# Kernel optimization log

Measured on AMD Instinct MI355X. Metric: run time of the kernel, lower is better.

## Reference

```python
import jax, jax.numpy as jnp
import numpy as np

B, T, C, H = 8, 2048, 768, 768

def setup_inputs() -> dict:
    key = jax.random.key(0)
    ks = jax.random.split(key, 7)
    s = 1.0 / np.sqrt(C)
    return {
        "visual_token": jax.random.normal(ks[0], (B, T, C), dtype=jnp.float32),
        "Wk": jax.random.normal(ks[1], (H, C), dtype=jnp.float32) * s,
        "bk": jax.random.normal(ks[2], (H,), dtype=jnp.float32) * s,
        "Wq": jax.random.normal(ks[3], (H, C), dtype=jnp.float32) * s,
        "bq": jax.random.normal(ks[4], (H,), dtype=jnp.float32) * s,
        "W1": jax.random.normal(ks[5], (C, C), dtype=jnp.float32) * s,
        "W2": jax.random.normal(ks[6], (C, C), dtype=jnp.float32) * s,
    }

def reference(visual_token, Wk, bk, Wq, bq, W1, W2):
    x = visual_token
    k = jnp.einsum('btc,hc->bth', x, Wk) + bk          # [B,T,H]
    q = jnp.einsum('btc,hc->bth', x, Wq) + bq          # [B,T,H]
    scores = jnp.einsum('bih,bjh->bij', k, q)          # K @ Q^T, unscaled
    attn = jax.nn.softmax(scores, axis=1)              # NOTE: softmax over dim=1 as in source
    p = x + jnp.einsum('bij,bjc->bic', attn, x)        # residual with value = input
    h = jnp.einsum('btc,dc->btd', p, W1)               # f_1 (no bias)
    h = jnp.einsum('btd,ed->bte', h, W2)               # f_2 (no bias)
    return p + jax.nn.relu(h)
```

## Files before the change

### kernel.cpp

```cpp
#include <hip/hip_runtime.h>

typedef float    f32x4 __attribute__((ext_vector_type(4)));
typedef _Float16 f16x8 __attribute__((ext_vector_type(8)));
typedef _Float16 f16x4 __attribute__((ext_vector_type(4)));

__device__ __forceinline__ void gload16(const void* g, void* l) {
  __builtin_amdgcn_global_load_lds(
      (__attribute__((address_space(1))) void*)(const void*)g,
      (__attribute__((address_space(3))) void*)l,
      16, 0, 0);
}

__device__ __forceinline__ void bounce_flush(const _Float16* lds, _Float16* gbase,
                                             int ldo, int t) {
#pragma unroll
  for (int it = 0; it < 8; ++it) {
    const int s = t + it * 512;
    const int R = s >> 5;
    const int C = (s & 31) * 8;
    const int wsrc = ((R >> 6) << 2) | (C >> 6);
    const f16x8 v = *(const f16x8*)(lds + wsrc * 4096 + (R & 63) * 64 +
                                    ((C & 63) ^ ((R & 12) << 2)));
    *(f16x8*)(gbase + (size_t)R * ldo + C) = v;
  }
}

template <int EPI>
__global__ __launch_bounds__(512, 4) void gemm_kt(
    const _Float16* __restrict__ A, size_t sA, int lda,
    const _Float16* __restrict__ B, size_t sB, int ldb,
    float* __restrict__ out0, _Float16* __restrict__ out1,
    float* __restrict__ out2,
    size_t sO, int ldo,
    const float* __restrict__ bias,
    const float* __restrict__ resid,
    const _Float16* __restrict__ residh,
    const _Float16* __restrict__ cf,
    int K) {
  __shared__ _Float16 lds[3 * 12288];
  __shared__ _Float16 clds[(EPI == 6) ? 4096 : 1];

  const int gx = gridDim.x, gy = gridDim.y;
  const int nblk = gx * gy * gridDim.z;
  int lin = (blockIdx.z * gy + blockIdx.y) * gx + blockIdx.x;
  lin = (lin & 7) * (nblk >> 3) + (lin >> 3);
  const int b  = lin / (gx * gy);
  const int r2 = lin - b * gx * gy;
  const int m0 = (r2 / gx) * 128;
  const int n0 = (r2 - (r2 / gx) * gx) * 256;

  const int t = threadIdx.x, lane = t & 63, w = t >> 6;
  const int wr = w >> 2;
  const int wc = w & 3;
  const int lr = lane & 15, lq = lane >> 4;

  const _Float16* Ab = A + (size_t)b * sA;
  const _Float16* Bb = B + (size_t)b * sB;

  const int arow = t >> 2;
  const int acol = ((t & 3) ^ ((arow >> 1) & 3)) * 8;
  const _Float16* a_src  = Ab + (size_t)(m0 + arow) * lda + acol;
  const _Float16* b_src0 = Bb + (size_t)(n0 + arow) * ldb + acol;
  const _Float16* b_src1 = b_src0 + (size_t)128 * ldb;
  const int a_dst  = t * 8;
  const int b_dst0 = 4096 + t * 8;
  const int b_dst1 = 4096 + (t + 512) * 8;

  const int swz  = ((lr >> 1) & 3) << 3;
  const int koff = (lq * 8) ^ swz;
  const int a_rd = (wr * 64 + lr) * 32 + koff;
  const int b_rd = 4096 + (wc * 64 + lr) * 32 + koff;

  f32x4 acc[4][4];
#pragma unroll
  for (int f = 0; f < 4; ++f)
#pragma unroll
    for (int j = 0; j < 4; ++j) acc[f][j] = (f32x4){0.f, 0.f, 0.f, 0.f};

  const int NT = K >> 5;

  if constexpr (EPI == 6)
    gload16(cf + ((size_t)b * 32 + (m0 >> 6)) * 2048 + t * 8, clds + t * 8);
  gload16(a_src,       lds + a_dst);
  gload16(b_src0,      lds + b_dst0);
  gload16(b_src1,      lds + b_dst1);
  gload16(a_src  + 32, lds + 12288 + a_dst);
  gload16(b_src0 + 32, lds + 12288 + b_dst0);
  gload16(b_src1 + 32, lds + 12288 + b_dst1);

  int buf = 0;
  for (int kt = 0; kt < NT; ++kt) {
    if (kt + 1 < NT) asm volatile("s_waitcnt vmcnt(3)" ::: "memory");
    else             asm volatile("s_waitcnt vmcnt(0)" ::: "memory");
    __builtin_amdgcn_s_barrier();
    __builtin_amdgcn_sched_barrier(0);

    const _Float16* lb = lds + buf * 12288;
    const int nb = (buf + 2 >= 3) ? buf - 1 : buf + 2;
    _Float16* ln = lds + nb * 12288;

    f16x8 af[4], bf[4], cv;
    if constexpr (EPI == 6)
      cv = *(const f16x8*)(clds + wr * 2048 + kt * 32 + lq * 8);
#pragma unroll
    for (int f = 0; f < 4; ++f) {
      af[f] = *(const f16x8*)(lb + a_rd + f * 512);
      if constexpr (EPI == 6) af[f] = af[f] * cv;
    }
#pragma unroll
    for (int j = 0; j < 4; ++j) bf[j] = *(const f16x8*)(lb + b_rd + j * 512);
    if (kt + 2 < NT) {
      const int ko = (kt + 2) * 32;
      gload16(a_src  + ko, ln + a_dst);
      gload16(b_src0 + ko, ln + b_dst0);
      gload16(b_src1 + ko, ln + b_dst1);
    }
    __builtin_amdgcn_s_setprio(1);
#pragma unroll
    for (int f = 0; f < 4; ++f)
#pragma unroll
      for (int j = 0; j < 4; ++j)
        acc[f][j] = __builtin_amdgcn_mfma_f32_16x16x32_f16(af[f], bf[j], acc[f][j], 0, 0, 0);
    __builtin_amdgcn_s_setprio(0);
    __builtin_amdgcn_sched_barrier(0);
    buf = (buf + 1 >= 3) ? 0 : buf + 1;
  }

  if constexpr (EPI == 0 || EPI == 4 || EPI == 6) {
    __syncthreads();
    _Float16* breg = lds + w * 4096;
    if constexpr (EPI == 4) {
#pragma unroll
      for (int j = 0; j < 4; ++j) {
        float m = -3.4e38f;
#pragma unroll
        for (int f = 0; f < 4; ++f)
#pragma unroll
          for (int r = 0; r < 4; ++r) m = fmaxf(m, acc[f][j][r]);
#pragma unroll
        for (int d = 16; d <= 32; d <<= 1) m = fmaxf(m, __shfl_xor(m, d, 64));
        float Z = 0.f;
        const int cb = ((j ^ lq) << 4) + lr;
#pragma unroll
        for (int f = 0; f < 4; ++f)
#pragma unroll
          for (int r = 0; r < 4; ++r) {
            const _Float16 eh = (_Float16)__expf(acc[f][j][r] - m);
            breg[(f * 16 + lq * 4 + r) * 64 + cb] = eh;
            Z += (float)eh;
          }
#pragma unroll
        for (int d = 16; d <= 32; d <<= 1) Z += __shfl_xor(Z, d, 64);
        if (lq == 0) {
          const int chunk = (m0 >> 6) + wr;
          const int col = n0 + wc * 64 + j * 16 + lr;
          const size_t sidx = ((size_t)b * 32 + chunk) * 2048 + col;
          out0[sidx] = m;
          out2[sidx] = Z;
        }
      }
    } else {
#pragma unroll
      for (int f = 0; f < 4; ++f)
#pragma unroll
        for (int j = 0; j < 4; ++j) {
          const int cb = ((j ^ lq) << 4) + lr;
#pragma unroll
          for (int r = 0; r < 4; ++r) {
            float v = acc[f][j][r];
            if constexpr (EPI == 0) {
              if (bias) v += bias[n0 + wc * 64 + j * 16 + lr];
            } else {
              const int row = m0 + wr * 64 + f * 16 + lq * 4 + r;
              const int col = n0 + wc * 64 + j * 16 + lr;
              v += resid[(size_t)b * sO + (size_t)row * ldo + col];
            }
            breg[(f * 16 + lq * 4 + r) * 64 + cb] = (_Float16)v;
          }
        }
    }
    __syncthreads();
    bounce_flush(lds, out1 + (size_t)b * sO + (size_t)m0 * ldo + n0, ldo, t);
  } else {
#pragma unroll
    for (int f = 0; f < 4; ++f)
#pragma unroll
      for (int j = 0; j < 4; ++j)
#pragma unroll
        for (int r = 0; r < 4; ++r) {
          const int row = m0 + wr * 64 + f * 16 + lq * 4 + r;
          const int col = n0 + wc * 64 + j * 16 + lr;
          const size_t oidx = (size_t)b * sO + (size_t)row * ldo + col;
          const float v = acc[f][j][r];
          out0[oidx] = (float)residh[oidx] + (v > 0.f ? v : 0.f);
        }
  }
}

__global__ __launch_bounds__(256) void wconv(
    const float* __restrict__ Wk, const float* __restrict__ Wq,
    const float* __restrict__ W1, const float* __restrict__ W2,
    _Float16* __restrict__ Wkqf, _Float16* __restrict__ W1f,
    _Float16* __restrict__ W2f,
    const float* __restrict__ bk, const float* __restrict__ bq,
    float* __restrict__ bkq) {
  const int by = blockIdx.y;
  const long i = (long)blockIdx.x * 256 + threadIdx.x;
  if (by == 4) {
    if (i < 768) bkq[i] = bk[i];
    else if (i < 1536) bkq[i] = bq[i - 768];
    return;
  }
  const float* in = (by == 0) ? Wk : (by == 1) ? Wq : (by == 2) ? W1 : W2;
  _Float16* outp = (by == 0) ? Wkqf : (by == 1) ? (Wkqf + 589824)
                  : (by == 2) ? W1f : W2f;
  f32x4 v0 = *(const f32x4*)(in + i * 8);
  f32x4 v1 = *(const f32x4*)(in + i * 8 + 4);
  f16x8 o;
  o[0] = (_Float16)v0[0]; o[1] = (_Float16)v0[1]; o[2] = (_Float16)v0[2]; o[3] = (_Float16)v0[3];
  o[4] = (_Float16)v1[0]; o[5] = (_Float16)v1[1]; o[6] = (_Float16)v1[2]; o[7] = (_Float16)v1[3];
  *(f16x8*)(outp + i * 8) = o;
}

__global__ __launch_bounds__(256) void col_final(const float* __restrict__ pm,
                                                 const float* __restrict__ pZ,
                                                 _Float16* __restrict__ c) {
  const int b = blockIdx.z;
  const int col = blockIdx.x * 256 + threadIdx.x;
  float mv[32];
  float m = -3.4e38f;
#pragma unroll
  for (int k = 0; k < 32; ++k) {
    mv[k] = pm[((size_t)b * 32 + k) * 2048 + col];
    m = fmaxf(m, mv[k]);
  }
  float Z = 0.f;
#pragma unroll
  for (int k = 0; k < 32; ++k)
    Z += pZ[((size_t)b * 32 + k) * 2048 + col] * __expf(mv[k] - m);
  const float rZ = 1.f / Z;
#pragma unroll
  for (int k = 0; k < 32; ++k)
    c[((size_t)b * 32 + k) * 2048 + col] = (_Float16)(__expf(mv[k] - m) * rZ);
}

__global__ void xprep(const float* __restrict__ x, _Float16* __restrict__ xf,
                      _Float16* __restrict__ xT) {
  __shared__ float tile[32][33];
  const int b = blockIdx.z;
  const int c0 = blockIdx.x * 32, j0 = blockIdx.y * 32;
  const float* xb = x + (size_t)b * 2048 * 768;
  const int tx = threadIdx.x, ty = threadIdx.y;
#pragma unroll
  for (int dy = 0; dy < 32; dy += 8)
    tile[ty + dy][tx] = xb[(size_t)(j0 + ty + dy) * 768 + c0 + tx];
  __syncthreads();
  {
    const int u = ty * 32 + tx;
    const int row = u >> 3, c4 = (u & 7) * 4;
    f16x4 o;
#pragma unroll
    for (int q = 0; q < 4; ++q) o[q] = (_Float16)tile[row][c4 + q];
    *(f16x4*)(xf + ((size_t)b * 2048 + j0 + row) * 768 + c0 + c4) = o;
  }
  _Float16* xTb = xT + (size_t)b * 768 * 2048;
#pragma unroll
  for (int dy = 0; dy < 32; dy += 8)
    xTb[(size_t)(c0 + ty + dy) * 2048 + j0 + tx] = (_Float16)tile[tx][ty + dy];
}

extern "C" void kernel_launch(void* const* d_in, const int* in_sizes, int n_in,
                              void* d_out, int out_size, void* d_ws, size_t ws_size,
                              hipStream_t stream) {
  const float* x  = (const float*)d_in[0];
  const float* Wk = (const float*)d_in[1];
  const float* bk = (const float*)d_in[2];
  const float* Wq = (const float*)d_in[3];
  const float* bq = (const float*)d_in[4];
  const float* W1 = (const float*)d_in[5];
  const float* W2 = (const float*)d_in[6];
  float* out = (float*)d_out;

  char* ws = (char*)d_ws;
  size_t off = 0;
  auto alloc = [&](size_t bytes) -> char* {
    char* p = ws + off;
    off += (bytes + 255) & ~(size_t)255;
    return p;
  };
  _Float16* xf = (_Float16*)alloc(25165824);
  _Float16* kq = (_Float16*)alloc(50331648);
  _Float16* Wf = (_Float16*)alloc(4718592);
  _Float16* E  = (_Float16*)alloc(67108864);
  _Float16* xT = (_Float16*)alloc(25165824);
  float*    pm = (float*)alloc(2097152);
  float*    pZ = (float*)alloc(2097152);
  float*    bkq  = (float*)alloc(6144);

  _Float16* Wkqf = Wf;
  _Float16* W1f  = Wf + 2 * 589824;
  _Float16* W2f  = Wf + 3 * 589824;
  _Float16* pf16 = kq;
  _Float16* cT   = kq + 12582912;
  _Float16* hf16 = kq + 12582912;

  const size_t sKQ = (size_t)2048 * 1536;
  const size_t sS  = (size_t)2048 * 2048;
  const size_t sKV = (size_t)2048 * 768;

  xprep<<<dim3(24, 64, 8), dim3(32, 8), 0, stream>>>(x, xf, xT);
  wconv<<<dim3(288, 5), 256, 0, stream>>>(Wk, Wq, W1, W2, Wkqf, W1f, W2f,
                                          bk, bq, bkq);

  gemm_kt<0><<<dim3(6, 128, 1), 512, 0, stream>>>(xf, 0, 768, Wkqf, 0, 768,
                                                  nullptr, kq, nullptr, 0, 1536,
                                                  bkq, nullptr, nullptr, nullptr, 768);

  gemm_kt<4><<<dim3(8, 16, 8), 512, 0, stream>>>(kq, sKQ, 1536, kq + 768, sKQ, 1536,
                                                 pm, E, pZ, sS, 2048,
                                                 nullptr, nullptr, nullptr, nullptr, 768);
  col_final<<<dim3(8, 1, 8), 256, 0, stream>>>(pm, pZ, cT);

  gemm_kt<6><<<dim3(3, 16, 8), 512, 0, stream>>>(E, sS, 2048, xT, sKV, 2048,
                                                 nullptr, pf16, nullptr, sKV, 768,
                                                 nullptr, x, nullptr, cT, 2048);

  gemm_kt<0><<<dim3(3, 128, 1), 512, 0, stream>>>(pf16, 0, 768, W1f, 0, 768,
                                                  nullptr, hf16, nullptr, 0, 768,
                                                  nullptr, nullptr, nullptr, nullptr, 768);

  gemm_kt<3><<<dim3(3, 128, 1), 512, 0, stream>>>(hf16, 0, 768, W2f, 0, 768,
                                                  out, nullptr, nullptr, 0, 768,
                                                  nullptr, nullptr, pf16, nullptr, 768);
}
```

Measured before the change: 264.0 us.

## Replace score GEMM with dedicated 256x256-tile kernel with split-phase pipelining

Moves the K·Q^T score GEMM with its fused exp/partial-max/partial-sum epilogue out of the generic 128x256 gemm_kt into a new epass256 kernel that uses 256x256 tiles. Each wave now computes 8x4 MFMA fragments, and the K-loop is split into two halves so LDS fragment loads and global-to-LDS prefetches overlap the MFMAs, with explicit waitcnt and barriers between them. The larger tile raises arithmetic intensity and reduces reloads of K and Q. In exchange it uses more registers and LDS, runs at occupancy 2, and launches only 512 blocks.

```diff
diff --git a/kernel.cpp b/kernel.cpp
--- a/kernel.cpp
+++ b/kernel.cpp
@@ -30,7 +30,6 @@
     const _Float16* __restrict__ A, size_t sA, int lda,
     const _Float16* __restrict__ B, size_t sB, int ldb,
     float* __restrict__ out0, _Float16* __restrict__ out1,
-    float* __restrict__ out2,
     size_t sO, int ldo,
     const float* __restrict__ bias,
     const float* __restrict__ resid,
@@ -50,8 +49,7 @@
   const int n0 = (r2 - (r2 / gx) * gx) * 256;
 
   const int t = threadIdx.x, lane = t & 63, w = t >> 6;
-  const int wr = w >> 2;
-  const int wc = w & 3;
+  const int wr = w >> 2, wc = w & 3;
   const int lr = lane & 15, lq = lane >> 4;
 
   const _Float16* Ab = A + (size_t)b * sA;
@@ -126,59 +124,27 @@
     buf = (buf + 1 >= 3) ? 0 : buf + 1;
   }
 
-  if constexpr (EPI == 0 || EPI == 4 || EPI == 6) {
+  if constexpr (EPI == 0 || EPI == 6) {
     __syncthreads();
     _Float16* breg = lds + w * 4096;
-    if constexpr (EPI == 4) {
+#pragma unroll
+    for (int f = 0; f < 4; ++f)
 #pragma unroll
       for (int j = 0; j < 4; ++j) {
-        float m = -3.4e38f;
-#pragma unroll
-        for (int f = 0; f < 4; ++f)
-#pragma unroll
-          for (int r = 0; r < 4; ++r) m = fmaxf(m, acc[f][j][r]);
-#pragma unroll
-        for (int d = 16; d <= 32; d <<= 1) m = fmaxf(m, __shfl_xor(m, d, 64));
-        float Z = 0.f;
         const int cb = ((j ^ lq) << 4) + lr;
 #pragma unroll
-        for (int f = 0; f < 4; ++f)
-#pragma unroll
-          for (int r = 0; r < 4; ++r) {
-            const _Float16 eh = (_Float16)__expf(acc[f][j][r] - m);
-            breg[(f * 16 + lq * 4 + r) * 64 + cb] = eh;
-            Z += (float)eh;
+        for (int r = 0; r < 4; ++r) {
+          float v = acc[f][j][r];
+          if constexpr (EPI == 0) {
+            if (bias) v += bias[n0 + wc * 64 + j * 16 + lr];
+          } else {
+            const int row = m0 + wr * 64 + f * 16 + lq * 4 + r;
+            const int col = n0 + wc * 64 + j * 16 + lr;
+            v += resid[(size_t)b * sO + (size_t)row * ldo + col];
           }
-#pragma unroll
-        for (int d = 16; d <= 32; d <<= 1) Z += __shfl_xor(Z, d, 64);
-        if (lq == 0) {
-          const int chunk = (m0 >> 6) + wr;
-          const int col = n0 + wc * 64 + j * 16 + lr;
-          const size_t sidx = ((size_t)b * 32 + chunk) * 2048 + col;
-          out0[sidx] = m;
-          out2[sidx] = Z;
+          breg[(f * 16 + lq * 4 + r) * 64 + cb] = (_Float16)v;
         }
       }
-    } else {
-#pragma unroll
-      for (int f = 0; f < 4; ++f)
-#pragma unroll
-        for (int j = 0; j < 4; ++j) {
-          const int cb = ((j ^ lq) << 4) + lr;
-#pragma unroll
-          for (int r = 0; r < 4; ++r) {
-            float v = acc[f][j][r];
-            if constexpr (EPI == 0) {
-              if (bias) v += bias[n0 + wc * 64 + j * 16 + lr];
-            } else {
-              const int row = m0 + wr * 64 + f * 16 + lq * 4 + r;
-              const int col = n0 + wc * 64 + j * 16 + lr;
-              v += resid[(size_t)b * sO + (size_t)row * ldo + col];
-            }
-            breg[(f * 16 + lq * 4 + r) * 64 + cb] = (_Float16)v;
-          }
-        }
-    }
     __syncthreads();
     bounce_flush(lds, out1 + (size_t)b * sO + (size_t)m0 * ldo + n0, ldo, t);
   } else {
@@ -194,6 +160,172 @@
           const float v = acc[f][j][r];
           out0[oidx] = (float)residh[oidx] + (v > 0.f ? v : 0.f);
         }
+  }
+}
+
+__global__ __launch_bounds__(512, 2) void epass256(
+    const _Float16* __restrict__ A, const _Float16* __restrict__ B,
+    float* __restrict__ pm, float* __restrict__ pZ,
+    _Float16* __restrict__ E) {
+  __shared__ _Float16 lds3[3 * 16384];
+
+  const int gx = 8, gy = 8;
+  const int nblk = 512;
+  int lin = (blockIdx.z * gy + blockIdx.y) * gx + blockIdx.x;
+  lin = (lin & 7) * (nblk >> 3) + (lin >> 3);
+  const int b  = lin >> 6;
+  const int r2 = lin & 63;
+  const int m0 = (r2 >> 3) * 256;
+  const int n0 = (r2 & 7) * 256;
+
+  const int t = threadIdx.x, lane = t & 63, w = t >> 6;
+  const int wr = w >> 2, wc = w & 3;
+  const int lr = lane & 15, lq = lane >> 4;
+
+  const _Float16* Ab = A + (size_t)b * 2048 * 1536;
+  const _Float16* Bb = B + (size_t)b * 2048 * 1536;
+
+  const int arow = t >> 2;
+  const int acol = ((t & 3) ^ ((arow >> 1) & 3)) * 8;
+  const _Float16* a_src0 = Ab + (size_t)(m0 + arow) * 1536 + acol;
+  const _Float16* a_src1 = a_src0 + (size_t)128 * 1536;
+  const _Float16* b_src0 = Bb + (size_t)(n0 + arow) * 1536 + acol;
+  const _Float16* b_src1 = b_src0 + (size_t)128 * 1536;
+  const int a_d0 = t * 8, a_d1 = (t + 512) * 8;
+  const int b_d0 = 8192 + t * 8, b_d1 = 8192 + (t + 512) * 8;
+
+  const int swz  = ((lr >> 1) & 3) << 3;
+  const int koff = (lq * 8) ^ swz;
+  const int a_rd = (wr * 128 + lr) * 32 + koff;
+  const int b_rd = 8192 + (wc * 64 + lr) * 32 + koff;
+
+  f32x4 acc[8][4];
+#pragma unroll
+  for (int f = 0; f < 8; ++f)
+#pragma unroll
+    for (int j = 0; j < 4; ++j) acc[f][j] = (f32x4){0.f, 0.f, 0.f, 0.f};
+
+  const int NT = 24;
+
+  gload16(a_src0, lds3 + a_d0);
+  gload16(a_src1, lds3 + a_d1);
+  gload16(b_src0, lds3 + b_d0);
+  gload16(b_src1, lds3 + b_d1);
+  gload16(a_src0 + 32, lds3 + 16384 + a_d0);
+  gload16(a_src1 + 32, lds3 + 16384 + a_d1);
+  gload16(b_src0 + 32, lds3 + 16384 + b_d0);
+  gload16(b_src1 + 32, lds3 + 16384 + b_d1);
+  asm volatile("s_waitcnt vmcnt(4)" ::: "memory");
+  __builtin_amdgcn_s_barrier();
+  __builtin_amdgcn_sched_barrier(0);
+
+  f16x8 afc[4], afb[4], bfc[4], afn[4], bfn[4];
+#pragma unroll
+  for (int f = 0; f < 4; ++f) afc[f] = *(const f16x8*)(lds3 + a_rd + f * 512);
+#pragma unroll
+  for (int j = 0; j < 4; ++j) bfc[j] = *(const f16x8*)(lds3 + b_rd + j * 512);
+
+  for (int kt = 0; kt < NT; ++kt) {
+    const _Float16* lb = lds3 + (kt % 3) * 16384;
+    const _Float16* lnx = lds3 + ((kt + 1) % 3) * 16384;
+    _Float16* lst = lds3 + ((kt + 2) % 3) * 16384;
+    const bool st2 = (kt + 2 < NT), nx = (kt + 1 < NT);
+    const int ko = (kt + 2) * 32;
+
+    if (st2) {
+      gload16(a_src0 + ko, lst + a_d0);
+      gload16(a_src1 + ko, lst + a_d1);
+    }
+#pragma unroll
+    for (int f = 0; f < 4; ++f) afb[f] = *(const f16x8*)(lb + a_rd + (4 + f) * 512);
+    __builtin_amdgcn_s_setprio(1);
+#pragma unroll
+    for (int f = 0; f < 4; ++f)
+#pragma unroll
+      for (int j = 0; j < 4; ++j)
+        acc[f][j] = __builtin_amdgcn_mfma_f32_16x16x32_f16(afc[f], bfc[j], acc[f][j], 0, 0, 0);
+    __builtin_amdgcn_s_setprio(0);
+    asm volatile("s_waitcnt lgkmcnt(0)" ::: "memory");
+    __builtin_amdgcn_s_barrier();
+    __builtin_amdgcn_sched_barrier(0);
+
+    if (st2) {
+      gload16(b_src0 + ko, lst + b_d0);
+      gload16(b_src1 + ko, lst + b_d1);
+    }
+    if (nx) {
+      if (st2) asm volatile("s_waitcnt vmcnt(4)" ::: "memory");
+      else     asm volatile("s_waitcnt vmcnt(0)" ::: "memory");
+      __builtin_amdgcn_sched_barrier(0);
+#pragma unroll
+      for (int f = 0; f < 4; ++f) afn[f] = *(const f16x8*)(lnx + a_rd + f * 512);
+#pragma unroll
+      for (int j = 0; j < 4; ++j) bfn[j] = *(const f16x8*)(lnx + b_rd + j * 512);
+    }
+    __builtin_amdgcn_s_setprio(1);
+#pragma unroll
+    for (int f = 0; f < 4; ++f)
+#pragma unroll
+      for (int j = 0; j < 4; ++j)
+        acc[4 + f][j] = __builtin_amdgcn_mfma_f32_16x16x32_f16(afb[f], bfc[j], acc[4 + f][j], 0, 0, 0);
+    __builtin_amdgcn_s_setprio(0);
+    asm volatile("s_waitcnt lgkmcnt(0)" ::: "memory");
+    __builtin_amdgcn_s_barrier();
+    __builtin_amdgcn_sched_barrier(0);
+    if (nx) {
+#pragma unroll
+      for (int f = 0; f < 4; ++f) afc[f] = afn[f];
+#pragma unroll
+      for (int j = 0; j < 4; ++j) bfc[j] = bfn[j];
+    }
+  }
+
+  _Float16* breg = lds3 + w * 4096;
+#pragma unroll
+  for (int h = 0; h < 2; ++h) {
+    if (h == 1) __syncthreads();
+#pragma unroll
+    for (int j = 0; j < 4; ++j) {
+      float m = -3.4e38f;
+#pragma unroll
+      for (int f = 0; f < 4; ++f)
+#pragma unroll
+        for (int r = 0; r < 4; ++r) m = fmaxf(m, acc[h * 4 + f][j][r]);
+#pragma unroll
+      for (int d = 16; d <= 32; d <<= 1) m = fmaxf(m, __shfl_xor(m, d, 64));
+      float Z = 0.f;
+      const int cb = ((j ^ lq) << 4) + lr;
+#pragma unroll
+      for (int f = 0; f < 4; ++f)
+#pragma unroll
+        for (int r = 0; r < 4; ++r) {
+          const _Float16 eh = (_Float16)__expf(acc[h * 4 + f][j][r] - m);
+          breg[(f * 16 + lq * 4 + r) * 64 + cb] = eh;
+          Z += (float)eh;
+        }
+#pragma unroll
+      for (int d = 16; d <= 32; d <<= 1) Z += __shfl_xor(Z, d, 64);
+      if (lq == 0) {
+        const int chunk = (m0 >> 6) + wr * 2 + h;
+        const int col = n0 + wc * 64 + j * 16 + lr;
+        const size_t sidx = ((size_t)b * 32 + chunk) * 2048 + col;
+        pm[sidx] = m;
+        pZ[sidx] = Z;
+      }
+    }
+    __syncthreads();
+#pragma unroll
+    for (int it = 0; it < 8; ++it) {
+      const int s = t + it * 512;
+      const int Rp = s >> 5;
+      const int C  = (s & 31) * 8;
+      const int wsrc = ((Rp >> 6) << 2) | (C >> 6);
+      const int rl = Rp & 63;
+      const f16x8 v = *(const f16x8*)(lds3 + wsrc * 4096 + rl * 64 +
+                                      ((C & 63) ^ (((rl >> 2) & 3) << 4)));
+      const int grow = m0 + (Rp >> 6) * 128 + h * 64 + rl;
+      *(f16x8*)(E + (size_t)b * 2048 * 2048 + (size_t)grow * 2048 + n0 + C) = v;
+    }
   }
 }
 
@@ -313,23 +445,21 @@
                                           bk, bq, bkq);
 
   gemm_kt<0><<<dim3(6, 128, 1), 512, 0, stream>>>(xf, 0, 768, Wkqf, 0, 768,
-                                                  nullptr, kq, nullptr, 0, 1536,
+                                                  nullptr, kq, 0, 1536,
                                                   bkq, nullptr, nullptr, nullptr, 768);
 
-  gemm_kt<4><<<dim3(8, 16, 8), 512, 0, stream>>>(kq, sKQ, 1536, kq + 768, sKQ, 1536,
-                                                 pm, E, pZ, sS, 2048,
-                                                 nullptr, nullptr, nullptr, nullptr, 768);
+  epass256<<<dim3(8, 8, 8), 512, 0, stream>>>(kq, kq + 768, pm, pZ, E);
   col_final<<<dim3(8, 1, 8), 256, 0, stream>>>(pm, pZ, cT);
 
   gemm_kt<6><<<dim3(3, 16, 8), 512, 0, stream>>>(E, sS, 2048, xT, sKV, 2048,
-                                                 nullptr, pf16, nullptr, sKV, 768,
+                                                 nullptr, pf16, sKV, 768,
                                                  nullptr, x, nullptr, cT, 2048);
 
   gemm_kt<0><<<dim3(3, 128, 1), 512, 0, stream>>>(pf16, 0, 768, W1f, 0, 768,
-                                                  nullptr, hf16, nullptr, 0, 768,
+                                                  nullptr, hf16, 0, 768,
                                                   nullptr, nullptr, nullptr, nullptr, 768);
 
   gemm_kt<3><<<dim3(3, 128, 1), 512, 0, stream>>>(hf16, 0, 768, W2f, 0, 768,
-                                                  out, nullptr, nullptr, 0, 768,
+                                                  out, nullptr, 0, 768,
                                                   nullptr, nullptr, pf16, nullptr, 768);
 }
```

Measured after the change: 266.0 us. Within noise of the previous version (+0.8%).

## Fold Wq^T Wk into one projection and drop bias terms invariant under softmax

Applied to the files above, without the earlier changes.

Rewrites scores = (xWk^T+bk)(xWq^T+bq)^T as x G x^T plus a per-row term u = x·(Wk^T bq), using G = Wq^T Wk precomputed by a small GEMM. Terms that are constant along the softmax axis (dim 1 over rows i), such as those involving bk, are dropped. The KQ projection GEMM shrinks from 1536 to 768 output columns, and the scores GEMM reads xf directly as its B operand. In exchange it adds weight-prep kernels (transpose, G GEMM, wu, u) and changes fp16 rounding, because G is stored in fp16.

```diff
diff --git a/kernel.cpp b/kernel.cpp
--- a/kernel.cpp
+++ b/kernel.cpp
@@ -43,15 +43,14 @@
   const int gx = gridDim.x, gy = gridDim.y;
   const int nblk = gx * gy * gridDim.z;
   int lin = (blockIdx.z * gy + blockIdx.y) * gx + blockIdx.x;
-  lin = (lin & 7) * (nblk >> 3) + (lin >> 3);
+  if (!(nblk & 7)) lin = (lin & 7) * (nblk >> 3) + (lin >> 3);
   const int b  = lin / (gx * gy);
   const int r2 = lin - b * gx * gy;
   const int m0 = (r2 / gx) * 128;
   const int n0 = (r2 - (r2 / gx) * gx) * 256;
 
   const int t = threadIdx.x, lane = t & 63, w = t >> 6;
-  const int wr = w >> 2;
-  const int wc = w & 3;
+  const int wr = w >> 2, wc = w & 3;
   const int lr = lane & 15, lq = lane >> 4;
 
   const _Float16* Ab = A + (size_t)b * sA;
@@ -130,13 +129,19 @@
     __syncthreads();
     _Float16* breg = lds + w * 4096;
     if constexpr (EPI == 4) {
+      float uu[4][4];
+#pragma unroll
+      for (int f = 0; f < 4; ++f)
+#pragma unroll
+        for (int r = 0; r < 4; ++r)
+          uu[f][r] = bias[(size_t)b * 2048 + m0 + wr * 64 + f * 16 + lq * 4 + r];
 #pragma unroll
       for (int j = 0; j < 4; ++j) {
         float m = -3.4e38f;
 #pragma unroll
         for (int f = 0; f < 4; ++f)
 #pragma unroll
-          for (int r = 0; r < 4; ++r) m = fmaxf(m, acc[f][j][r]);
+          for (int r = 0; r < 4; ++r) m = fmaxf(m, acc[f][j][r] + uu[f][r]);
 #pragma unroll
         for (int d = 16; d <= 32; d <<= 1) m = fmaxf(m, __shfl_xor(m, d, 64));
         float Z = 0.f;
@@ -145,7 +150,7 @@
         for (int f = 0; f < 4; ++f)
 #pragma unroll
           for (int r = 0; r < 4; ++r) {
-            const _Float16 eh = (_Float16)__expf(acc[f][j][r] - m);
+            const _Float16 eh = (_Float16)__expf(acc[f][j][r] + uu[f][r] - m);
             breg[(f * 16 + lq * 4 + r) * 64 + cb] = eh;
             Z += (float)eh;
           }
@@ -197,29 +202,72 @@
   }
 }
 
-__global__ __launch_bounds__(256) void wconv(
-    const float* __restrict__ Wk, const float* __restrict__ Wq,
-    const float* __restrict__ W1, const float* __restrict__ W2,
-    _Float16* __restrict__ Wkqf, _Float16* __restrict__ W1f,
-    _Float16* __restrict__ W2f,
-    const float* __restrict__ bk, const float* __restrict__ bq,
-    float* __restrict__ bkq) {
-  const int by = blockIdx.y;
+__global__ __launch_bounds__(256) void wconv(const float* __restrict__ W1,
+                                             const float* __restrict__ W2,
+                                             _Float16* __restrict__ W1f,
+                                             _Float16* __restrict__ W2f) {
   const long i = (long)blockIdx.x * 256 + threadIdx.x;
-  if (by == 4) {
-    if (i < 768) bkq[i] = bk[i];
-    else if (i < 1536) bkq[i] = bq[i - 768];
-    return;
-  }
-  const float* in = (by == 0) ? Wk : (by == 1) ? Wq : (by == 2) ? W1 : W2;
-  _Float16* outp = (by == 0) ? Wkqf : (by == 1) ? (Wkqf + 589824)
-                  : (by == 2) ? W1f : W2f;
+  const float* in = blockIdx.y ? W2 : W1;
+  _Float16* outp  = blockIdx.y ? W2f : W1f;
   f32x4 v0 = *(const f32x4*)(in + i * 8);
   f32x4 v1 = *(const f32x4*)(in + i * 8 + 4);
   f16x8 o;
   o[0] = (_Float16)v0[0]; o[1] = (_Float16)v0[1]; o[2] = (_Float16)v0[2]; o[3] = (_Float16)v0[3];
   o[4] = (_Float16)v1[0]; o[5] = (_Float16)v1[1]; o[6] = (_Float16)v1[2]; o[7] = (_Float16)v1[3];
   *(f16x8*)(outp + i * 8) = o;
+}
+
+__global__ void wprepT(const float* __restrict__ Wk, const float* __restrict__ Wq,
+                       _Float16* __restrict__ WkT, _Float16* __restrict__ WqT) {
+  __shared__ float tile[32][33];
+  const float* src = blockIdx.z ? Wq : Wk;
+  _Float16*    dst = blockIdx.z ? WqT : WkT;
+  const int c0 = blockIdx.x * 32, h0 = blockIdx.y * 32;
+  const int tx = threadIdx.x, ty = threadIdx.y;
+#pragma unroll
+  for (int dy = 0; dy < 32; dy += 8)
+    tile[ty + dy][tx] = src[(size_t)(h0 + ty + dy) * 768 + c0 + tx];
+  __syncthreads();
+#pragma unroll
+  for (int dy = 0; dy < 32; dy += 8)
+    dst[(size_t)(c0 + ty + dy) * 768 + h0 + tx] = (_Float16)tile[tx][ty + dy];
+}
+
+__global__ __launch_bounds__(256) void wuk(const float* __restrict__ Wk,
+                                           const float* __restrict__ bq,
+                                           float* __restrict__ wu) {
+  const int c = blockIdx.x * 256 + threadIdx.x;
+  float s = 0.f;
+  for (int h = 0; h < 768; ++h) s += Wk[(size_t)h * 768 + c] * bq[h];
+  wu[c] = s;
+}
+
+__global__ __launch_bounds__(256) void uvk(const _Float16* __restrict__ xf,
+                                           const float* __restrict__ wu,
+                                           float* __restrict__ u) {
+  __shared__ float wus[768];
+  for (int i = threadIdx.x; i < 768; i += 256) wus[i] = wu[i];
+  __syncthreads();
+  const int w = threadIdx.x >> 6, lane = threadIdx.x & 63;
+  const int wid = blockIdx.x * 4 + w;
+#pragma unroll 1
+  for (int rr = 0; rr < 16; ++rr) {
+    const int row = wid * 16 + rr;
+    float s = 0.f;
+    {
+      const f16x8 xv = *(const f16x8*)(xf + (size_t)row * 768 + lane * 8);
+#pragma unroll
+      for (int e = 0; e < 8; ++e) s += (float)xv[e] * wus[lane * 8 + e];
+    }
+    if (lane < 32) {
+      const f16x8 xv = *(const f16x8*)(xf + (size_t)row * 768 + (lane + 64) * 8);
+#pragma unroll
+      for (int e = 0; e < 8; ++e) s += (float)xv[e] * wus[(lane + 64) * 8 + e];
+    }
+#pragma unroll
+    for (int d = 1; d < 64; d <<= 1) s += __shfl_xor(s, d, 64);
+    if (lane == 0) u[row] = s;
+  }
 }
 
 __global__ __launch_bounds__(256) void col_final(const float* __restrict__ pm,
@@ -280,6 +328,7 @@
   const float* W1 = (const float*)d_in[5];
   const float* W2 = (const float*)d_in[6];
   float* out = (float*)d_out;
+  (void)bk;
 
   char* ws = (char*)d_ws;
   size_t off = 0;
@@ -289,36 +338,45 @@
     return p;
   };
   _Float16* xf = (_Float16*)alloc(25165824);
-  _Float16* kq = (_Float16*)alloc(50331648);
-  _Float16* Wf = (_Float16*)alloc(4718592);
+  _Float16* zb = (_Float16*)alloc(50331648);
+  _Float16* Wf = (_Float16*)alloc(5898240);
   _Float16* E  = (_Float16*)alloc(67108864);
   _Float16* xT = (_Float16*)alloc(25165824);
   float*    pm = (float*)alloc(2097152);
   float*    pZ = (float*)alloc(2097152);
-  float*    bkq  = (float*)alloc(6144);
-
-  _Float16* Wkqf = Wf;
-  _Float16* W1f  = Wf + 2 * 589824;
-  _Float16* W2f  = Wf + 3 * 589824;
-  _Float16* pf16 = kq;
-  _Float16* cT   = kq + 12582912;
-  _Float16* hf16 = kq + 12582912;
-
-  const size_t sKQ = (size_t)2048 * 1536;
+  float*    wu = (float*)alloc(3072);
+  float*    ub = (float*)alloc(65536);
+
+  _Float16* W1f = Wf;
+  _Float16* W2f = Wf + 589824;
+  _Float16* WkT = Wf + 2 * 589824;
+  _Float16* WqT = Wf + 3 * 589824;
+  _Float16* G   = Wf + 4 * 589824;
+  _Float16* pf16 = zb;
+  _Float16* cT   = zb + 12582912;
+  _Float16* hf16 = zb + 12582912;
+
   const size_t sS  = (size_t)2048 * 2048;
   const size_t sKV = (size_t)2048 * 768;
 
   xprep<<<dim3(24, 64, 8), dim3(32, 8), 0, stream>>>(x, xf, xT);
-  wconv<<<dim3(288, 5), 256, 0, stream>>>(Wk, Wq, W1, W2, Wkqf, W1f, W2f,
-                                          bk, bq, bkq);
-
-  gemm_kt<0><<<dim3(6, 128, 1), 512, 0, stream>>>(xf, 0, 768, Wkqf, 0, 768,
-                                                  nullptr, kq, nullptr, 0, 1536,
-                                                  bkq, nullptr, nullptr, nullptr, 768);
-
-  gemm_kt<4><<<dim3(8, 16, 8), 512, 0, stream>>>(kq, sKQ, 1536, kq + 768, sKQ, 1536,
+  wconv<<<dim3(288, 2), 256, 0, stream>>>(W1, W2, W1f, W2f);
+  wprepT<<<dim3(24, 24, 2), dim3(32, 8), 0, stream>>>(Wk, Wq, WkT, WqT);
+  wuk<<<3, 256, 0, stream>>>(Wk, bq, wu);
+
+  gemm_kt<0><<<dim3(3, 6, 1), 512, 0, stream>>>(WqT, 0, 768, WkT, 0, 768,
+                                                nullptr, G, nullptr, 0, 768,
+                                                nullptr, nullptr, nullptr, nullptr, 768);
+
+  uvk<<<256, 256, 0, stream>>>(xf, wu, ub);
+
+  gemm_kt<0><<<dim3(3, 128, 1), 512, 0, stream>>>(xf, 0, 768, G, 0, 768,
+                                                  nullptr, zb, nullptr, 0, 768,
+                                                  nullptr, nullptr, nullptr, nullptr, 768);
+
+  gemm_kt<4><<<dim3(8, 16, 8), 512, 0, stream>>>(zb, sKV, 768, xf, sKV, 768,
                                                  pm, E, pZ, sS, 2048,
-                                                 nullptr, nullptr, nullptr, nullptr, 768);
+                                                 ub, nullptr, nullptr, nullptr, 768);
   col_final<<<dim3(8, 1, 8), 256, 0, stream>>>(pm, pZ, cT);
 
   gemm_kt<6><<<dim3(3, 16, 8), 512, 0, stream>>>(E, sS, 2048, xT, sKV, 2048,
```

Result: slower. 315.5 us (+19.5%).
